# Performance work log

Hardware: AMD Instinct MI355X
Metric: run time of the kernel (lower is better)

The kernel has to match this reference:

```python
import jax, jax.numpy as jnp
import numpy as np
from jax import lax

B, L, H, E, V = 16, 128, 1024, 512, 32000
MAX_LENGTH = 128
SOS_INDEX = 1
NUM_LAYERS = 2


def setup_inputs() -> dict:
    key = jax.random.key(0)
    ks = jax.random.split(key, 16)
    inp = {}
    inp['input_tensor'] = jax.random.randint(ks[0], (B, L), 0, V)
    inp['target_tensor'] = jax.random.randint(ks[1], (B, L), 0, V)
    inp['true_sample'] = 1
    s = lambda k, shape, fan: jax.random.normal(k, shape, jnp.float32) / np.float32(np.sqrt(fan))
    inp['embedding'] = jax.random.normal(ks[2], (V, E), jnp.float32) * 0.02
    inp['enc_W'] = s(ks[3], (E, H), E)
    inp['enc_b'] = jnp.zeros((H,), jnp.float32)
    inp['Wih0'] = s(ks[4], (E, 3 * H), E)
    inp['Whh0'] = s(ks[5], (H, 3 * H), H)
    inp['bih0'] = jnp.zeros((3 * H,), jnp.float32)
    inp['bhh0'] = jnp.zeros((3 * H,), jnp.float32)
    inp['Wih1'] = s(ks[6], (H, 3 * H), H)
    inp['Whh1'] = s(ks[7], (H, 3 * H), H)
    inp['bih1'] = jnp.zeros((3 * H,), jnp.float32)
    inp['bhh1'] = jnp.zeros((3 * H,), jnp.float32)
    inp['W_out'] = s(ks[8], (2 * H, V), 2 * H)
    inp['b_out'] = jnp.zeros((V,), jnp.float32)
    return inp


def _gru_cell(x, h, Wih, Whh, bih, bhh):
    gx = x @ Wih + bih
    gh = h @ Whh + bhh
    xr, xz, xn = jnp.split(gx, 3, axis=-1)
    hr, hz, hn = jnp.split(gh, 3, axis=-1)
    r = jax.nn.sigmoid(xr + hr)
    z = jax.nn.sigmoid(xz + hz)
    n = jnp.tanh(xn + r * hn)
    return (1.0 - z) * n + z * h


def _forward(input_tensor, true_sample, embedding, enc_W, enc_b,
             Wih0, Whh0, bih0, bhh0, Wih1, Whh1, bih1, bhh1, W_out, b_out):
    batch_size, input_length = input_tensor.shape
    target_length = input_length
    # Encoder: embed + per-timestep projection -> [B, L, H]
    enc_emb = embedding[input_tensor]
    enc_hidden = jnp.tanh(enc_emb @ enc_W + enc_b)
    enc_hidden_t = jnp.transpose(enc_hidden, (1, 0, 2))  # [L, B, H]
    # Pad at the front to max_length (mirrors the copy loop)
    encoder_outputs = jnp.zeros((MAX_LENGTH, batch_size, H), enc_hidden.dtype)
    encoder_outputs = encoder_outputs.at[MAX_LENGTH - input_length:].set(enc_hidden_t)
    # Decoder initial hidden: last encoder state stacked over layers
    h_init = enc_hidden_t[-1]  # [B, H]
    # NOTE: original never updates decoder_input inside the loop -> constant SOS
    x0 = jnp.broadcast_to(embedding[SOS_INDEX], (batch_size, E))
    inv_sqrt_h = np.float32(1.0 / np.sqrt(H))

    def step(carry, _):
        h0, h1 = carry
        h0 = _gru_cell(x0, h0, Wih0, Whh0, bih0, bhh0)
        h1 = _gru_cell(h0, h1, Wih1, Whh1, bih1, bhh1)
        scores = jnp.einsum('bh,lbh->bl', h1, encoder_outputs) * inv_sqrt_h
        attn = jax.nn.softmax(scores, axis=-1)
        ctx = jnp.einsum('bl,lbh->bh', attn, encoder_outputs)
        logits = jnp.concatenate([h1, ctx], axis=-1) @ W_out + b_out
        return (h0, h1), jax.nn.sigmoid(logits)

    _, probs = lax.scan(step, (h_init, h_init), None, length=target_length)
    decoder_outputs = jnp.transpose(probs, (1, 0, 2))  # [B, T, V]
    # Scalar gather: p[b,w] = decoder_outputs[b, w, input_tensor[b, w]]
    out_probabilities = jnp.take_along_axis(decoder_outputs, input_tensor[..., None], axis=2)[..., 0]
    target = jnp.full(input_tensor.shape, np.float32(int(true_sample)), jnp.float32)
    p = jnp.clip(out_probabilities, 1e-12, 1.0 - 1e-7)
    bce = -(target * jnp.log(p) + (1.0 - target) * jnp.log1p(-p))
    loss = jnp.mean(bce) / np.float32(batch_size)
    return loss, out_probabilities


def reference(input_tensor, target_tensor, true_sample, embedding, enc_W, enc_b,
              Wih0, Whh0, bih0, bhh0, Wih1, Whh1, bih1, bhh1, W_out, b_out):
    return _forward(input_tensor, true_sample, embedding, enc_W, enc_b,
                    Wih0, Whh0, bih0, bhh0, Wih1, Whh1, bih1, bhh1, W_out, b_out)
```

## Files before the change

### kernel.cpp

```cpp
#include <hip/hip_runtime.h>
#include <math.h>

#define BB 16
#define LL 128
#define HH 1024
#define EE 512
#define VV 32000
#define G3 3072
#define NBLK 256

__device__ __forceinline__ float sigmoidf_(float x){ return 1.0f/(1.0f+expf(-x)); }

__device__ __forceinline__ float red64(float v){
  v += __shfl_xor(v, 1, 64); v += __shfl_xor(v, 2, 64);
  v += __shfl_xor(v, 4, 64); v += __shfl_xor(v, 8, 64);
  v += __shfl_xor(v, 16, 64); v += __shfl_xor(v, 32, 64);
  return v;
}
__device__ __forceinline__ float red32(float v){
  v += __shfl_xor(v, 1, 64); v += __shfl_xor(v, 2, 64);
  v += __shfl_xor(v, 4, 64); v += __shfl_xor(v, 8, 64);
  v += __shfl_xor(v, 16, 64);
  return v;
}

__global__ void k_rowidx(const int* __restrict__ inp, int* __restrict__ idx){
  int r = blockIdx.x*256 + threadIdx.x;
  if (r < 2048){ int l = r >> 4, b = r & 15; idx[r] = inp[b*LL + l]; }
}

template<int ACT, int KK>
__global__ __launch_bounds__(256) void k_gemm(const float* __restrict__ A, const int* __restrict__ rowidx,
                       const float* __restrict__ Bm, const float* __restrict__ bias,
                       float* __restrict__ C, int N){
  constexpr int KS = (KK==512)?9:10;
  __shared__ float As[32*KK];
  const int tid = threadIdx.x;
  const int r0 = blockIdx.x*32;
  const int c  = blockIdx.y*512 + (tid<<1);
  for (int i = tid; i < 32*KK; i += 256){
    int rr = i >> KS;
    int row = r0 + rr;
    int arow = rowidx ? rowidx[row] : row;
    int kk = i - (rr<<KS);
    As[i] = A[(size_t)arow*KK + kk];
  }
  __syncthreads();
  float2 acc[32];
  #pragma unroll
  for (int r=0;r<32;r++){ acc[r].x=0.f; acc[r].y=0.f; }
  for (int k=0;k<KK;k++){
    const float2 w = *(const float2*)(Bm + (size_t)k*N + c);
    #pragma unroll
    for (int r=0;r<32;r++){
      float a = As[(r<<KS)+k];
      acc[r].x = fmaf(a,w.x,acc[r].x);
      acc[r].y = fmaf(a,w.y,acc[r].y);
    }
  }
  const float2 bv = *(const float2*)(bias + c);
  #pragma unroll
  for (int r=0;r<32;r++){
    float x = acc[r].x + bv.x, y = acc[r].y + bv.y;
    if (ACT==1){ x = tanhf(x); y = tanhf(y); }
    *(float2*)(C + (size_t)(r0+r)*N + c) = make_float2(x,y);
  }
}

__global__ __launch_bounds__(512,1) void k_chains(
    const float* enclast, float* H0all, float* H1all,
    const float* __restrict__ Whh0, const float* __restrict__ Whh1,
    const float* __restrict__ Wih0, const float* __restrict__ Wih1,
    const float* __restrict__ emb,
    const float* __restrict__ bih0, const float* __restrict__ bhh0,
    const float* __restrict__ bhh1, const float* __restrict__ bih1,
    int* flags, int* go)
{
  __shared__ float w0l[12][1024];
  __shared__ float w1l[12][1024];
  __shared__ float wil[12][1024];
  __shared__ float gxbuf[16*12];
  const int tid  = threadIdx.x;
  const int jb   = blockIdx.x << 2;
  const int waveid = tid >> 6;
  const int cgA = waveid >> 2;
  const int bgA = waveid & 3;
  const int kgA = tid & 63;
  const int koffA = kgA << 2;
  const int b0A = bgA << 2;
  const int cgB = waveid >> 1;
  const int bgB = ((waveid & 1) << 1) | ((tid >> 5) & 1);
  const int kgB = tid & 31;
  const int koffB = kgB << 2;
  const int b0B = bgB << 2;
  const int mB  = cgB >> 1;

  const bool pwA = (kgA < 8);
  const int  jlA = (cgA << 1) + (kgA & 1);
  const int  jpA = jb + jlA;
  const int  biA = (kgA >> 1) & 3;
  const int  bA  = b0A + biA;
  const bool pwB = (cgB >= 2) && (kgB < 8);
  const int  jlB = ((cgB & 1) << 1) + (kgB & 1);
  const int  jpB = jb + jlB;
  const int  biB = (kgB >> 1) & 3;
  const int  bB  = b0B + biB;

  float g0r=0.f, g0z=0.f, g0n=0.f;
  {
    for (int idx = tid; idx < 1536; idx += 512){
      int g = idx >> 9, k = idx & 511;
      float4 a = *(const float4*)(Wih0 + (size_t)k*G3 + g*1024 + jb);
      w0l[g*4+0][k]=a.x; w0l[g*4+1][k]=a.y; w0l[g*4+2][k]=a.z; w0l[g*4+3][k]=a.w;
    }
    __syncthreads();
    const float* e1 = emb + EE;
    float ag[6];
    #pragma unroll
    for (int cl=0;cl<6;cl++) ag[cl]=0.f;
    #pragma unroll
    for (int u=0;u<2;u++){
      float4 e = *(const float4*)(e1 + u*256 + koffA);
      #pragma unroll
      for (int cl=0;cl<6;cl++){
        const int gc = ((cl>>1)<<2) + (cgA<<1) + (cl&1);
        const float4 w = *(const float4*)(&w0l[gc][u*256 + koffA]);
        float v = ag[cl];
        v=fmaf(w.x,e.x,v); v=fmaf(w.y,e.y,v); v=fmaf(w.z,e.z,v); v=fmaf(w.w,e.w,v);
        ag[cl]=v;
      }
    }
    #pragma unroll
    for (int cl=0;cl<6;cl++) ag[cl] = red64(ag[cl]);
    if (pwA){
      const int jj = kgA & 1;
      g0r = (jj ? ag[1] : ag[0]) + bih0[jpA];
      g0z = (jj ? ag[3] : ag[2]) + bih0[1024+jpA];
      g0n = (jj ? ag[5] : ag[4]) + bih0[2048+jpA];
    }
    __syncthreads();
  }

  for (int idx = tid; idx < 3072; idx += 512){
    int g = idx >> 10, k = idx & 1023;
    float4 a = *(const float4*)(Whh0 + (size_t)k*G3 + g*1024 + jb);
    w0l[g*4+0][k]=a.x; w0l[g*4+1][k]=a.y; w0l[g*4+2][k]=a.z; w0l[g*4+3][k]=a.w;
    float4 d = *(const float4*)(Whh1 + (size_t)k*G3 + g*1024 + jb);
    w1l[g*4+0][k]=d.x; w1l[g*4+1][k]=d.y; w1l[g*4+2][k]=d.z; w1l[g*4+3][k]=d.w;
    float4 e = *(const float4*)(Wih1 + (size_t)k*G3 + g*1024 + jb);
    wil[g*4+0][k]=e.x; wil[g*4+1][k]=e.y; wil[g*4+2][k]=e.z; wil[g*4+3][k]=e.w;
  }
  float b0rA=0.f,b0zA=0.f,b0nA=0.f;
  if (pwA){ b0rA = bhh0[jpA]; b0zA = bhh0[1024+jpA]; b0nA = bhh0[2048+jpA]; }
  float birB=0.f,bizB=0.f,binB=0.f,b1rB=0.f,b1zB=0.f,b1nB=0.f;
  if (pwB){
    birB = bih1[jpB]; bizB = bih1[1024+jpB]; binB = bih1[2048+jpB];
    b1rB = bhh1[jpB]; b1zB = bhh1[1024+jpB]; b1nB = bhh1[2048+jpB];
  }
  __syncthreads();

  const int myflag = (int)blockIdx.x * 32;

  for (int t = 0; t <= LL; ++t){
    if (t >= 1){
      if (blockIdx.x == 0){
        if (tid < 256){
          while (__hip_atomic_load(&flags[tid*32], __ATOMIC_RELAXED,
                                   __HIP_MEMORY_SCOPE_AGENT) < t)
            __builtin_amdgcn_s_sleep(1);
        }
        __syncthreads();
        if (tid == 0)
          __hip_atomic_store(go, t, __ATOMIC_RELAXED, __HIP_MEMORY_SCOPE_AGENT);
      } else {
        if (tid == 0){
          while (__hip_atomic_load(go, __ATOMIC_RELAXED,
                                   __HIP_MEMORY_SCOPE_AGENT) < t)
            __builtin_amdgcn_s_sleep(1);
        }
        __syncthreads();
      }
    }

    if (t >= 1){
      const float* hp0 = H0all + (size_t)(t-1)*(BB*HH);
      const float* hp1 = (t==1) ? enclast : (H1all + (size_t)(t-2)*(BB*HH));
      const float* hr  = mB ? hp1 : hp0;
      float hprev1 = 0.f;
      if (pwB) hprev1 = hp1[(size_t)bB*HH + jpB];

      float accB[6][4];
      #pragma unroll
      for (int cl=0;cl<6;cl++)
        #pragma unroll
        for (int bi=0;bi<4;bi++) accB[cl][bi]=0.f;

      #pragma unroll
      for (int u=0;u<8;u++){
        float4 h4[4];
        #pragma unroll
        for (int bi=0;bi<4;bi++)
          h4[bi] = *(const float4*)(hr + (size_t)(b0B+bi)*HH + u*128 + koffB);
        #pragma unroll
        for (int cl=0;cl<6;cl++){
          const int gc = ((cl>>1)<<2) + ((cgB&1)<<1) + (cl&1);
          const float4 w = mB ? *(const float4*)(&w1l[gc][u*128 + koffB])
                              : *(const float4*)(&wil[gc][u*128 + koffB]);
          #pragma unroll
          for (int bi=0;bi<4;bi++){
            float v = accB[cl][bi];
            v=fmaf(w.x,h4[bi].x,v); v=fmaf(w.y,h4[bi].y,v);
            v=fmaf(w.z,h4[bi].z,v); v=fmaf(w.w,h4[bi].w,v);
            accB[cl][bi]=v;
          }
        }
      }
      #pragma unroll
      for (int cl=0;cl<6;cl++)
        #pragma unroll
        for (int bi=0;bi<4;bi++) accB[cl][bi] = red32(accB[cl][bi]);

      if (mB == 0){
        #pragma unroll
        for (int cl=0;cl<6;cl++){
          if (kgB == cl){
            const int g = cl >> 1;
            const int jl = ((cgB&1)<<1) + (cl&1);
            #pragma unroll
            for (int bi=0;bi<4;bi++)
              gxbuf[(b0B+bi)*12 + g*4 + jl] = accB[cl][bi];
          }
        }
      }
      __syncthreads();
      if (pwB){
        float ghr=0.f, ghz=0.f, ghn=0.f;
        #pragma unroll
        for (int jj=0;jj<2;jj++)
          #pragma unroll
          for (int ii=0;ii<4;ii++){
            bool sel = ((kgB&1)==jj) & (biB==ii);
            ghr = sel ? accB[jj][ii]   : ghr;
            ghz = sel ? accB[2+jj][ii] : ghz;
            ghn = sel ? accB[4+jj][ii] : ghn;
          }
        float gxr = gxbuf[bB*12 + 0*4 + jlB];
        float gxz = gxbuf[bB*12 + 1*4 + jlB];
        float gxn = gxbuf[bB*12 + 2*4 + jlB];
        float r = sigmoidf_(gxr + birB + ghr + b1rB);
        float z = sigmoidf_(gxz + bizB + ghz + b1zB);
        float n = tanhf    (gxn + binB + r*(ghn + b1nB));
        float hnew = (1.f-z)*n + z*hprev1;
        __hip_atomic_store((int*)&H1all[(size_t)(t-1)*(BB*HH) + (size_t)bB*HH + jpB],
                           __float_as_int(hnew),
                           __ATOMIC_RELAXED, __HIP_MEMORY_SCOPE_AGENT);
      }
    }

    if (t < LL){
      const float* hp0 = (t==0) ? enclast : (H0all + (size_t)(t-1)*(BB*HH));
      float hprev0 = 0.f;
      if (pwA) hprev0 = hp0[(size_t)bA*HH + jpA];

      float acc0[6][4];
      #pragma unroll
      for (int cl=0;cl<6;cl++)
        #pragma unroll
        for (int bi=0;bi<4;bi++) acc0[cl][bi]=0.f;

      #pragma unroll
      for (int u=0;u<4;u++){
        float4 h4[4];
        #pragma unroll
        for (int bi=0;bi<4;bi++)
          h4[bi] = *(const float4*)(hp0 + (size_t)(b0A+bi)*HH + u*256 + koffA);
        #pragma unroll
        for (int cl=0;cl<6;cl++){
          const int gc = ((cl>>1)<<2) + (cgA<<1) + (cl&1);
          const float4 w = *(const float4*)(&w0l[gc][u*256 + koffA]);
          #pragma unroll
          for (int bi=0;bi<4;bi++){
            float v = acc0[cl][bi];
            v=fmaf(w.x,h4[bi].x,v); v=fmaf(w.y,h4[bi].y,v);
            v=fmaf(w.z,h4[bi].z,v); v=fmaf(w.w,h4[bi].w,v);
            acc0[cl][bi]=v;
          }
        }
      }
      #pragma unroll
      for (int cl=0;cl<6;cl++)
        #pragma unroll
        for (int bi=0;bi<4;bi++) acc0[cl][bi] = red64(acc0[cl][bi]);

      if (pwA){
        float ghr=0.f, ghz=0.f, ghn=0.f;
        #pragma unroll
        for (int jj=0;jj<2;jj++)
          #pragma unroll
          for (int ii=0;ii<4;ii++){
            bool sel = ((kgA&1)==jj) & (biA==ii);
            ghr = sel ? acc0[jj][ii]   : ghr;
            ghz = sel ? acc0[2+jj][ii] : ghz;
            ghn = sel ? acc0[4+jj][ii] : ghn;
          }
        float r = sigmoidf_(g0r + ghr + b0rA);
        float z = sigmoidf_(g0z + ghz + b0zA);
        float n = tanhf    (g0n + r*(ghn + b0nA));
        float hnew = (1.f-z)*n + z*hprev0;
        __hip_atomic_store((int*)&H0all[(size_t)t*(BB*HH) + (size_t)bA*HH + jpA],
                           __float_as_int(hnew),
                           __ATOMIC_RELAXED, __HIP_MEMORY_SCOPE_AGENT);
      }
    }

    if (t < LL){
      asm volatile("s_waitcnt vmcnt(0)" ::: "memory");
      __syncthreads();
      if (tid == 0)
        __hip_atomic_store(&flags[myflag], t+1,
                           __ATOMIC_RELAXED, __HIP_MEMORY_SCOPE_AGENT);
    }
  }
}

__global__ __launch_bounds__(256) void k_attn(const float* __restrict__ enc, const float* __restrict__ H1,
                       float* __restrict__ ctx){
  __shared__ float h1s[8][HH];
  __shared__ float sc[8][LL];
  __shared__ float part[2][8][LL];
  const int tid = threadIdx.x;
  const int s0 = blockIdx.x*8, b = blockIdx.y;
  for (int i = tid; i < 8*HH; i += 256){
    int si = i >> 10, k = i & 1023;
    h1s[si][k] = H1[(size_t)(s0+si)*BB*HH + (size_t)b*HH + k];
  }
  __syncthreads();
  {
    const int l = tid & 127, half = tid >> 7;
    const float4* er = (const float4*)(enc + ((size_t)l*BB + b)*HH + half*512);
    float a[8];
    #pragma unroll
    for (int s=0;s<8;s++) a[s]=0.f;
    for (int q=0;q<128;q++){
      float4 e = er[q];
      #pragma unroll
      for (int s=0;s<8;s++){
        const float4 h = *(const float4*)(&h1s[s][half*512 + q*4]);
        a[s] += h.x*e.x + h.y*e.y + h.z*e.z + h.w*e.w;
      }
    }
    #pragma unroll
    for (int s=0;s<8;s++) part[half][s][l] = a[s];
  }
  __syncthreads();
  for (int p = tid; p < 1024; p += 256){
    int s = p >> 7, l = p & 127;
    sc[s][l] = (part[0][s][l] + part[1][s][l]) * 0.03125f;
  }
  __syncthreads();
  {
    int s = tid >> 5, lid = tid & 31;
    float v0 = sc[s][lid], v1 = sc[s][lid+32], v2 = sc[s][lid+64], v3 = sc[s][lid+96];
    float m = fmaxf(fmaxf(v0,v1),fmaxf(v2,v3));
    for (int off=16; off>=1; off>>=1) m = fmaxf(m, __shfl_xor(m, off, 32));
    float e0=__expf(v0-m), e1=__expf(v1-m), e2=__expf(v2-m), e3=__expf(v3-m);
    float ssum = e0+e1+e2+e3;
    for (int off=16; off>=1; off>>=1) ssum += __shfl_xor(ssum, off, 32);
    float inv = 1.0f/ssum;
    sc[s][lid]=e0*inv; sc[s][lid+32]=e1*inv; sc[s][lid+64]=e2*inv; sc[s][lid+96]=e3*inv;
  }
  __syncthreads();
  {
    float acc[4][8];
    #pragma unroll
    for (int q=0;q<4;q++)
      #pragma unroll
      for (int s=0;s<8;s++) acc[q][s]=0.f;
    for (int l=0;l<128;l++){
      const float* er = enc + ((size_t)l*BB + b)*HH + tid;
      float a[8];
      #pragma unroll
      for (int s=0;s<8;s++) a[s] = sc[s][l];
      #pragma unroll
      for (int q=0;q<4;q++){
        float e = er[q*256];
        #pragma unroll
        for (int s=0;s<8;s++) acc[q][s] = fmaf(a[s], e, acc[q][s]);
      }
    }
    #pragma unroll
    for (int s=0;s<8;s++)
      #pragma unroll
      for (int q=0;q<4;q++)
        ctx[(size_t)(s0+s)*BB*HH + (size_t)b*HH + tid + q*256] = acc[q][s];
  }
}

__global__ __launch_bounds__(256) void k_logit(const float* __restrict__ H1, const float* __restrict__ ctx,
                        const float* __restrict__ Wout, const float* __restrict__ bout,
                        const int* __restrict__ inp, const int* __restrict__ ts,
                        float* __restrict__ outp, float* __restrict__ bce){
  __shared__ float rbuf[256];
  const int i = blockIdx.x;
  const int b = i >> 7, t = i & 127;
  const int v = inp[b*LL + t];
  const int tid = threadIdx.x;
  const float* h1r = H1 + ((size_t)t*BB + b)*HH;
  const float* cxr = ctx + ((size_t)t*BB + b)*HH;
  float acc = 0.f;
  #pragma unroll
  for (int q=0;q<4;q++){
    int k = tid + q*256;
    acc = fmaf(h1r[k], Wout[(size_t)k*VV + v], acc);
  }
  #pragma unroll
  for (int q=0;q<4;q++){
    int k = tid + q*256;
    acc = fmaf(cxr[k], Wout[(size_t)(k+1024)*VV + v], acc);
  }
  rbuf[tid] = acc;
  __syncthreads();
  for (int s=128; s>0; s>>=1){
    if (tid < s) rbuf[tid] += rbuf[tid+s];
    __syncthreads();
  }
  if (tid==0){
    float logit = rbuf[0] + bout[v];
    float p = 1.0f/(1.0f + expf(-logit));
    outp[b*LL + t] = p;
    float pc = fminf(fmaxf(p, 1e-12f), 1.0f - 1e-7f);
    float tg = (float)ts[0];
    bce[i] = -(tg*logf(pc) + (1.0f-tg)*log1pf(-pc));
  }
}

__global__ void k_loss(const float* __restrict__ bce, float* __restrict__ out0){
  __shared__ float rbuf[256];
  int tid = threadIdx.x;
  float s = 0.f;
  for (int i = tid; i < 2048; i += 256) s += bce[i];
  rbuf[tid] = s; __syncthreads();
  for (int st=128; st>0; st>>=1){
    if (tid<st) rbuf[tid]+=rbuf[tid+st];
    __syncthreads();
  }
  if (tid==0) out0[0] = rbuf[0] * (1.0f/(2048.0f*16.0f));
}

extern "C" void kernel_launch(void* const* d_in, const int* in_sizes, int n_in,
                              void* d_out, int out_size, void* d_ws, size_t ws_size,
                              hipStream_t stream){
  (void)in_sizes; (void)n_in; (void)out_size; (void)ws_size;
  const int*   inp   = (const int*)d_in[0];
  const int*   ts    = (const int*)d_in[2];
  const float* emb   = (const float*)d_in[3];
  const float* encW  = (const float*)d_in[4];
  const float* encb  = (const float*)d_in[5];
  const float* Wih0  = (const float*)d_in[6];
  const float* Whh0  = (const float*)d_in[7];
  const float* bih0  = (const float*)d_in[8];
  const float* bhh0  = (const float*)d_in[9];
  const float* Wih1  = (const float*)d_in[10];
  const float* Whh1  = (const float*)d_in[11];
  const float* bih1  = (const float*)d_in[12];
  const float* bhh1  = (const float*)d_in[13];
  const float* Wout  = (const float*)d_in[14];
  const float* bout  = (const float*)d_in[15];
  float* out = (float*)d_out;

  float* ws      = (float*)d_ws;
  float* enc_out = ws;
  float* H0      = enc_out + 2097152;
  float* H1      = H0 + 2097152;
  float* GX1     = H1 + 2097152;
  float* CTX     = GX1 + 6291456;
  float* gx0     = CTX + 2097152;
  float* bceb    = gx0 + 3072;
  int*   rowidx  = (int*)(bceb + 2048);
  int*   flags   = rowidx + 2048;
  int*   go      = flags + 256*32;

  hipMemsetAsync(flags, 0, (256*32 + 32)*sizeof(int), stream);
  k_rowidx<<<8,256,0,stream>>>(inp, rowidx);
  k_gemm<1,512><<<dim3(64,2),256,0,stream>>>(emb, rowidx, encW, encb, enc_out, HH);

  const float* enclast = enc_out + (size_t)127*BB*HH;

  k_chains<<<NBLK,512,0,stream>>>(enclast, H0, H1, Whh0, Whh1, Wih0, Wih1, emb,
                                  bih0, bhh0, bhh1, bih1, flags, go);
  k_attn<<<dim3(16,16),256,0,stream>>>(enc_out, H1, CTX);
  k_logit<<<2048,256,0,stream>>>(H1, CTX, Wout, bout, inp, ts, out+1, bceb);
  k_loss<<<1,256,0,stream>>>(bceb, out);
}
```

Before: 2.070 ms.

## Store recurrent GRU weights as packed fp16 in LDS and use dot2 with 1024 threads

The persistent recurrent kernel now converts Whh0, Whh1, Wih1 and Wih0 slices to packed half pairs in shared memory. It computes the gate dot products with v_dot2_f32_f16, with hidden states also packed to fp16 on the fly. The block size doubles to 1024 threads and the work is remapped so each wave covers fewer batch rows per layer-0 group, halving LDS footprint and per-thread register accumulators. This targets the per-step latency of the serial 128-step chain, but it reduces precision of the recurrent matmuls to fp16 inputs, which may drift over many steps.

```diff
diff --git a/kernel.cpp b/kernel.cpp
--- a/kernel.cpp
+++ b/kernel.cpp
@@ -8,19 +8,24 @@
 #define VV 32000
 #define G3 3072
 #define NBLK 256
+#define KP 576
+
+typedef __fp16 h2t __attribute__((ext_vector_type(2)));
+typedef unsigned int uint_;
 
 __device__ __forceinline__ float sigmoidf_(float x){ return 1.0f/(1.0f+expf(-x)); }
 
+__device__ __forceinline__ uint_ pk16(float a, float b){
+  h2t h = __builtin_amdgcn_cvt_pkrtz(a, b);
+  return __builtin_bit_cast(uint_, h);
+}
+__device__ __forceinline__ void dot2(float& acc, uint_ w, uint_ h){
+  asm("v_dot2_f32_f16 %0, %1, %2, %0" : "+v"(acc) : "v"(w), "v"(h));
+}
 __device__ __forceinline__ float red64(float v){
   v += __shfl_xor(v, 1, 64); v += __shfl_xor(v, 2, 64);
   v += __shfl_xor(v, 4, 64); v += __shfl_xor(v, 8, 64);
   v += __shfl_xor(v, 16, 64); v += __shfl_xor(v, 32, 64);
-  return v;
-}
-__device__ __forceinline__ float red32(float v){
-  v += __shfl_xor(v, 1, 64); v += __shfl_xor(v, 2, 64);
-  v += __shfl_xor(v, 4, 64); v += __shfl_xor(v, 8, 64);
-  v += __shfl_xor(v, 16, 64);
   return v;
 }
 
@@ -67,7 +72,7 @@
   }
 }
 
-__global__ __launch_bounds__(512,1) void k_chains(
+__global__ __launch_bounds__(1024,1) void k_chains(
     const float* enclast, float* H0all, float* H1all,
     const float* __restrict__ Whh0, const float* __restrict__ Whh1,
     const float* __restrict__ Wih0, const float* __restrict__ Wih1,
@@ -76,42 +81,44 @@
     const float* __restrict__ bhh1, const float* __restrict__ bih1,
     int* flags, int* go)
 {
-  __shared__ float w0l[12][1024];
-  __shared__ float w1l[12][1024];
-  __shared__ float wil[12][1024];
+  __shared__ uint_ w0l[12][KP];
+  __shared__ uint_ w1l[12][KP];
+  __shared__ uint_ wil[12][KP];
   __shared__ float gxbuf[16*12];
   const int tid  = threadIdx.x;
   const int jb   = blockIdx.x << 2;
   const int waveid = tid >> 6;
-  const int cgA = waveid >> 2;
-  const int bgA = waveid & 3;
-  const int kgA = tid & 63;
-  const int koffA = kgA << 2;
-  const int b0A = bgA << 2;
-  const int cgB = waveid >> 1;
-  const int bgB = ((waveid & 1) << 1) | ((tid >> 5) & 1);
-  const int kgB = tid & 31;
-  const int koffB = kgB << 2;
+  const int lane = tid & 63;
+  const int cgA = waveid >> 3;
+  const int bgA = waveid & 7;
+  const int b0A = bgA << 1;
+  const int cgB = waveid >> 2;
+  const int mB  = cgB >> 1;
+  const int bgB = waveid & 3;
   const int b0B = bgB << 2;
-  const int mB  = cgB >> 1;
-
-  const bool pwA = (kgA < 8);
-  const int  jlA = (cgA << 1) + (kgA & 1);
+  const int koff = lane << 2;
+
+  const bool pwA = (lane < 4);
+  const int  jlA = (cgA << 1) + (lane & 1);
   const int  jpA = jb + jlA;
-  const int  biA = (kgA >> 1) & 3;
+  const int  biA = (lane >> 1) & 1;
   const int  bA  = b0A + biA;
-  const bool pwB = (cgB >= 2) && (kgB < 8);
-  const int  jlB = ((cgB & 1) << 1) + (kgB & 1);
+  const bool pwB = (mB == 1) && (lane < 8);
+  const int  jlB = ((cgB & 1) << 1) + (lane & 1);
   const int  jpB = jb + jlB;
-  const int  biB = (kgB >> 1) & 3;
+  const int  biB = (lane >> 1) & 3;
   const int  bB  = b0B + biB;
 
   float g0r=0.f, g0z=0.f, g0n=0.f;
   {
-    for (int idx = tid; idx < 1536; idx += 512){
-      int g = idx >> 9, k = idx & 511;
-      float4 a = *(const float4*)(Wih0 + (size_t)k*G3 + g*1024 + jb);
-      w0l[g*4+0][k]=a.x; w0l[g*4+1][k]=a.y; w0l[g*4+2][k]=a.z; w0l[g*4+3][k]=a.w;
+    for (int idx = tid; idx < 768; idx += 1024){
+      int g = idx >> 8, kp = idx & 255, k = kp << 1;
+      float4 a0 = *(const float4*)(Wih0 + (size_t)k*G3 + g*1024 + jb);
+      float4 a1 = *(const float4*)(Wih0 + (size_t)(k+1)*G3 + g*1024 + jb);
+      w0l[g*4+0][kp] = pk16(a0.x, a1.x);
+      w0l[g*4+1][kp] = pk16(a0.y, a1.y);
+      w0l[g*4+2][kp] = pk16(a0.z, a1.z);
+      w0l[g*4+3][kp] = pk16(a0.w, a1.w);
     }
     __syncthreads();
     const float* e1 = emb + EE;
@@ -120,20 +127,20 @@
     for (int cl=0;cl<6;cl++) ag[cl]=0.f;
     #pragma unroll
     for (int u=0;u<2;u++){
-      float4 e = *(const float4*)(e1 + u*256 + koffA);
+      const int k0 = u*256 + koff, kp0 = (k0 >> 1);
+      float4 e = *(const float4*)(e1 + k0);
+      uint_ e01 = pk16(e.x, e.y), e23 = pk16(e.z, e.w);
       #pragma unroll
       for (int cl=0;cl<6;cl++){
         const int gc = ((cl>>1)<<2) + (cgA<<1) + (cl&1);
-        const float4 w = *(const float4*)(&w0l[gc][u*256 + koffA]);
-        float v = ag[cl];
-        v=fmaf(w.x,e.x,v); v=fmaf(w.y,e.y,v); v=fmaf(w.z,e.z,v); v=fmaf(w.w,e.w,v);
-        ag[cl]=v;
+        dot2(ag[cl], w0l[gc][kp0],   e01);
+        dot2(ag[cl], w0l[gc][kp0+1], e23);
       }
     }
     #pragma unroll
     for (int cl=0;cl<6;cl++) ag[cl] = red64(ag[cl]);
     if (pwA){
-      const int jj = kgA & 1;
+      const int jj = lane & 1;
       g0r = (jj ? ag[1] : ag[0]) + bih0[jpA];
       g0z = (jj ? ag[3] : ag[2]) + bih0[1024+jpA];
       g0n = (jj ? ag[5] : ag[4]) + bih0[2048+jpA];
@@ -141,14 +148,32 @@
     __syncthreads();
   }
 
-  for (int idx = tid; idx < 3072; idx += 512){
-    int g = idx >> 10, k = idx & 1023;
-    float4 a = *(const float4*)(Whh0 + (size_t)k*G3 + g*1024 + jb);
-    w0l[g*4+0][k]=a.x; w0l[g*4+1][k]=a.y; w0l[g*4+2][k]=a.z; w0l[g*4+3][k]=a.w;
-    float4 d = *(const float4*)(Whh1 + (size_t)k*G3 + g*1024 + jb);
-    w1l[g*4+0][k]=d.x; w1l[g*4+1][k]=d.y; w1l[g*4+2][k]=d.z; w1l[g*4+3][k]=d.w;
-    float4 e = *(const float4*)(Wih1 + (size_t)k*G3 + g*1024 + jb);
-    wil[g*4+0][k]=e.x; wil[g*4+1][k]=e.y; wil[g*4+2][k]=e.z; wil[g*4+3][k]=e.w;
+  for (int idx = tid; idx < 1536; idx += 1024){
+    int g = idx >> 9, kp = idx & 511, k = kp << 1;
+    {
+      float4 a0 = *(const float4*)(Whh0 + (size_t)k*G3 + g*1024 + jb);
+      float4 a1 = *(const float4*)(Whh0 + (size_t)(k+1)*G3 + g*1024 + jb);
+      w0l[g*4+0][kp] = pk16(a0.x, a1.x);
+      w0l[g*4+1][kp] = pk16(a0.y, a1.y);
+      w0l[g*4+2][kp] = pk16(a0.z, a1.z);
+      w0l[g*4+3][kp] = pk16(a0.w, a1.w);
+    }
+    {
+      float4 a0 = *(const float4*)(Whh1 + (size_t)k*G3 + g*1024 + jb);
+      float4 a1 = *(const float4*)(Whh1 + (size_t)(k+1)*G3 + g*1024 + jb);
+      w1l[g*4+0][kp] = pk16(a0.x, a1.x);
+      w1l[g*4+1][kp] = pk16(a0.y, a1.y);
+      w1l[g*4+2][kp] = pk16(a0.z, a1.z);
+      w1l[g*4+3][kp] = pk16(a0.w, a1.w);
+    }
+    {
+      float4 a0 = *(const float4*)(Wih1 + (size_t)k*G3 + g*1024 + jb);
+      float4 a1 = *(const float4*)(Wih1 + (size_t)(k+1)*G3 + g*1024 + jb);
+      wil[g*4+0][kp] = pk16(a0.x, a1.x);
+      wil[g*4+1][kp] = pk16(a0.y, a1.y);
+      wil[g*4+2][kp] = pk16(a0.z, a1.z);
+      wil[g*4+3][kp] = pk16(a0.w, a1.w);
+    }
   }
   float b0rA=0.f,b0zA=0.f,b0nA=0.f;
   if (pwA){ b0rA = bhh0[jpA]; b0zA = bhh0[1024+jpA]; b0nA = bhh0[2048+jpA]; }
@@ -196,34 +221,36 @@
         for (int bi=0;bi<4;bi++) accB[cl][bi]=0.f;
 
       #pragma unroll
-      for (int u=0;u<8;u++){
-        float4 h4[4];
-        #pragma unroll
-        for (int bi=0;bi<4;bi++)
-          h4[bi] = *(const float4*)(hr + (size_t)(b0B+bi)*HH + u*128 + koffB);
+      for (int u=0;u<4;u++){
+        const int k0 = u*256 + koff, kp0 = (k0 >> 1);
+        uint_ hh[4][2];
+        #pragma unroll
+        for (int bi=0;bi<4;bi++){
+          float4 hv = *(const float4*)(hr + (size_t)(b0B+bi)*HH + k0);
+          hh[bi][0] = pk16(hv.x, hv.y);
+          hh[bi][1] = pk16(hv.z, hv.w);
+        }
         #pragma unroll
         for (int cl=0;cl<6;cl++){
           const int gc = ((cl>>1)<<2) + ((cgB&1)<<1) + (cl&1);
-          const float4 w = mB ? *(const float4*)(&w1l[gc][u*128 + koffB])
-                              : *(const float4*)(&wil[gc][u*128 + koffB]);
+          const uint_ w01 = mB ? w1l[gc][kp0]   : wil[gc][kp0];
+          const uint_ w23 = mB ? w1l[gc][kp0+1] : wil[gc][kp0+1];
           #pragma unroll
           for (int bi=0;bi<4;bi++){
-            float v = accB[cl][bi];
-            v=fmaf(w.x,h4[bi].x,v); v=fmaf(w.y,h4[bi].y,v);
-            v=fmaf(w.z,h4[bi].z,v); v=fmaf(w.w,h4[bi].w,v);
-            accB[cl][bi]=v;
+            dot2(accB[cl][bi], w01, hh[bi][0]);
+            dot2(accB[cl][bi], w23, hh[bi][1]);
           }
         }
       }
       #pragma unroll
       for (int cl=0;cl<6;cl++)
         #pragma unroll
-        for (int bi=0;bi<4;bi++) accB[cl][bi] = red32(accB[cl][bi]);
+        for (int bi=0;bi<4;bi++) accB[cl][bi] = red64(accB[cl][bi]);
 
       if (mB == 0){
         #pragma unroll
         for (int cl=0;cl<6;cl++){
-          if (kgB == cl){
+          if (lane == cl){
             const int g = cl >> 1;
             const int jl = ((cgB&1)<<1) + (cl&1);
             #pragma unroll
@@ -239,14 +266,14 @@
         for (int jj=0;jj<2;jj++)
           #pragma unroll
           for (int ii=0;ii<4;ii++){
-            bool sel = ((kgB&1)==jj) & (biB==ii);
+            bool sel = ((lane&1)==jj) & (biB==ii);
             ghr = sel ? accB[jj][ii]   : ghr;
             ghz = sel ? accB[2+jj][ii] : ghz;
             ghn = sel ? accB[4+jj][ii] : ghn;
           }
-        float gxr = gxbuf[bB*12 + 0*4 + jlB];
-        float gxz = gxbuf[bB*12 + 1*4 + jlB];
-        float gxn = gxbuf[bB*12 + 2*4 + jlB];
+        float gxr = gxbuf[bB*12 + 0 + jlB];
+        float gxz = gxbuf[bB*12 + 4 + jlB];
+        float gxn = gxbuf[bB*12 + 8 + jlB];
         float r = sigmoidf_(gxr + birB + ghr + b1rB);
         float z = sigmoidf_(gxz + bizB + ghz + b1zB);
         float n = tanhf    (gxn + binB + r*(ghn + b1nB));
@@ -262,43 +289,45 @@
       float hprev0 = 0.f;
       if (pwA) hprev0 = hp0[(size_t)bA*HH + jpA];
 
-      float acc0[6][4];
-      #pragma unroll
-      for (int cl=0;cl<6;cl++)
-        #pragma unroll
-        for (int bi=0;bi<4;bi++) acc0[cl][bi]=0.f;
+      float acc0[6][2];
+      #pragma unroll
+      for (int cl=0;cl<6;cl++){ acc0[cl][0]=0.f; acc0[cl][1]=0.f; }
 
       #pragma unroll
       for (int u=0;u<4;u++){
-        float4 h4[4];
-        #pragma unroll
-        for (int bi=0;bi<4;bi++)
-          h4[bi] = *(const float4*)(hp0 + (size_t)(b0A+bi)*HH + u*256 + koffA);
+        const int k0 = u*256 + koff, kp0 = (k0 >> 1);
+        uint_ hh[2][2];
+        #pragma unroll
+        for (int bi=0;bi<2;bi++){
+          float4 hv = *(const float4*)(hp0 + (size_t)(b0A+bi)*HH + k0);
+          hh[bi][0] = pk16(hv.x, hv.y);
+          hh[bi][1] = pk16(hv.z, hv.w);
+        }
         #pragma unroll
         for (int cl=0;cl<6;cl++){
           const int gc = ((cl>>1)<<2) + (cgA<<1) + (cl&1);
-          const float4 w = *(const float4*)(&w0l[gc][u*256 + koffA]);
+          const uint_ w01 = w0l[gc][kp0];
+          const uint_ w23 = w0l[gc][kp0+1];
           #pragma unroll
-          for (int bi=0;bi<4;bi++){
-            float v = acc0[cl][bi];
-            v=fmaf(w.x,h4[bi].x,v); v=fmaf(w.y,h4[bi].y,v);
-            v=fmaf(w.z,h4[bi].z,v); v=fmaf(w.w,h4[bi].w,v);
-            acc0[cl][bi]=v;
+          for (int bi=0;bi<2;bi++){
+            dot2(acc0[cl][bi], w01, hh[bi][0]);
+            dot2(acc0[cl][bi], w23, hh[bi][1]);
           }
         }
       }
       #pragma unroll
-      for (int cl=0;cl<6;cl++)
-        #pragma unroll
-        for (int bi=0;bi<4;bi++) acc0[cl][bi] = red64(acc0[cl][bi]);
+      for (int cl=0;cl<6;cl++){
+        acc0[cl][0] = red64(acc0[cl][0]);
+        acc0[cl][1] = red64(acc0[cl][1]);
+      }
 
       if (pwA){
         float ghr=0.f, ghz=0.f, ghn=0.f;
         #pragma unroll
         for (int jj=0;jj<2;jj++)
           #pragma unroll
-          for (int ii=0;ii<4;ii++){
-            bool sel = ((kgA&1)==jj) & (biA==ii);
+          for (int ii=0;ii<2;ii++){
+            bool sel = ((lane&1)==jj) & (biA==ii);
             ghr = sel ? acc0[jj][ii]   : ghr;
             ghz = sel ? acc0[2+jj][ii] : ghz;
             ghn = sel ? acc0[4+jj][ii] : ghn;
@@ -480,14 +509,14 @@
   int*   flags   = rowidx + 2048;
   int*   go      = flags + 256*32;
 
-  hipMemsetAsync(flags, 0, (256*32 + 32)*sizeof(int), stream);
+  (void)hipMemsetAsync(flags, 0, (256*32 + 32)*sizeof(int), stream);
   k_rowidx<<<8,256,0,stream>>>(inp, rowidx);
   k_gemm<1,512><<<dim3(64,2),256,0,stream>>>(emb, rowidx, encW, encb, enc_out, HH);
 
   const float* enclast = enc_out + (size_t)127*BB*HH;
 
-  k_chains<<<NBLK,512,0,stream>>>(enclast, H0, H1, Whh0, Whh1, Wih0, Wih1, emb,
-                                  bih0, bhh0, bhh1, bih1, flags, go);
+  k_chains<<<NBLK,1024,0,stream>>>(enclast, H0, H1, Whh0, Whh1, Wih0, Wih1, emb,
+                                   bih0, bhh0, bhh1, bih1, flags, go);
   k_attn<<<dim3(16,16),256,0,stream>>>(enc_out, H1, CTX);
   k_logit<<<2048,256,0,stream>>>(H1, CTX, Wout, bout, inp, ts, out+1, bceb);
   k_loss<<<1,256,0,stream>>>(bceb, out);
```

Result: slower. 2.812 ms (+35.9%).

## Split GRU layers into separate persistent block groups with fp16 dot2 for layer 1

Applied to the files above, without the earlier changes.

The persistent recurrence kernel is split into two groups of 256 blocks. One group runs layer 0 and the other runs layer 1, each with its own flag/go barrier, and layer 1 trails layer 0 by one step via the layer-0 go counter. Layer-1 weights are packed to fp16 pairs in shared memory and multiplied with v_dot2_f32_f16, so Wih1 and Whh1 fit in one 48 KB buffer alongside the layer split. The aim is to shorten the per-step critical path and shrink LDS per block so more blocks fit. The cost is lower precision in layer 1 and a dependence on all 512 blocks being co-resident, which risks deadlock.

```diff
diff --git a/kernel.cpp b/kernel.cpp
--- a/kernel.cpp
+++ b/kernel.cpp
@@ -9,8 +9,18 @@
 #define G3 3072
 #define NBLK 256
 
+typedef __fp16 h2t __attribute__((ext_vector_type(2)));
+typedef unsigned int uint_;
+
 __device__ __forceinline__ float sigmoidf_(float x){ return 1.0f/(1.0f+expf(-x)); }
 
+__device__ __forceinline__ uint_ pk16(float a, float b){
+  h2t h = __builtin_amdgcn_cvt_pkrtz(a, b);
+  return __builtin_bit_cast(uint_, h);
+}
+__device__ __forceinline__ void dot2(float& acc, uint_ w, uint_ h){
+  asm("v_dot2_f32_f16 %0, %1, %2, %0" : "+v"(acc) : "v"(w), "v"(h));
+}
 __device__ __forceinline__ float red64(float v){
   v += __shfl_xor(v, 1, 64); v += __shfl_xor(v, 2, 64);
   v += __shfl_xor(v, 4, 64); v += __shfl_xor(v, 8, 64);
@@ -74,117 +84,236 @@
     const float* __restrict__ emb,
     const float* __restrict__ bih0, const float* __restrict__ bhh0,
     const float* __restrict__ bhh1, const float* __restrict__ bih1,
-    int* flags, int* go)
+    int* flagsA, int* flagsB, int* goA, int* goB)
 {
-  __shared__ float w0l[12][1024];
-  __shared__ float w1l[12][1024];
-  __shared__ float wil[12][1024];
+  __shared__ uint_ wbuf[12][1024];
   __shared__ float gxbuf[16*12];
-  const int tid  = threadIdx.x;
-  const int jb   = blockIdx.x << 2;
+  float (*wf)[1024] = (float(*)[1024])wbuf;
+  const int tid = threadIdx.x;
   const int waveid = tid >> 6;
-  const int cgA = waveid >> 2;
-  const int bgA = waveid & 3;
-  const int kgA = tid & 63;
-  const int koffA = kgA << 2;
-  const int b0A = bgA << 2;
-  const int cgB = waveid >> 1;
-  const int bgB = ((waveid & 1) << 1) | ((tid >> 5) & 1);
-  const int kgB = tid & 31;
-  const int koffB = kgB << 2;
-  const int b0B = bgB << 2;
-  const int mB  = cgB >> 1;
-
-  const bool pwA = (kgA < 8);
-  const int  jlA = (cgA << 1) + (kgA & 1);
-  const int  jpA = jb + jlA;
-  const int  biA = (kgA >> 1) & 3;
-  const int  bA  = b0A + biA;
-  const bool pwB = (cgB >= 2) && (kgB < 8);
-  const int  jlB = ((cgB & 1) << 1) + (kgB & 1);
-  const int  jpB = jb + jlB;
-  const int  biB = (kgB >> 1) & 3;
-  const int  bB  = b0B + biB;
-
-  float g0r=0.f, g0z=0.f, g0n=0.f;
-  {
+  const bool isA = (blockIdx.x < NBLK);
+  const int bx = isA ? (int)blockIdx.x : ((int)blockIdx.x - NBLK);
+  const int jb = bx << 2;
+
+  if (isA){
+    const int cgA = waveid >> 2;
+    const int bgA = waveid & 3;
+    const int kgA = tid & 63;
+    const int koffA = kgA << 2;
+    const int b0A = bgA << 2;
+    const bool pwA = (kgA < 8);
+    const int jlA = (cgA << 1) + (kgA & 1);
+    const int jpA = jb + jlA;
+    const int biA = (kgA >> 1) & 3;
+    const int bA  = b0A + biA;
+
+    float g0r=0.f, g0z=0.f, g0n=0.f;
+    {
+      for (int idx = tid; idx < 1536; idx += 512){
+        int g = idx >> 9, k = idx & 511;
+        float4 a = *(const float4*)(Wih0 + (size_t)k*G3 + g*1024 + jb);
+        wf[g*4+0][k]=a.x; wf[g*4+1][k]=a.y; wf[g*4+2][k]=a.z; wf[g*4+3][k]=a.w;
+      }
+      __syncthreads();
+      const float* e1 = emb + EE;
+      float ag[6];
+      #pragma unroll
+      for (int cl=0;cl<6;cl++) ag[cl]=0.f;
+      #pragma unroll
+      for (int u=0;u<2;u++){
+        float4 e = *(const float4*)(e1 + u*256 + koffA);
+        #pragma unroll
+        for (int cl=0;cl<6;cl++){
+          const int gc = ((cl>>1)<<2) + (cgA<<1) + (cl&1);
+          const float4 w = *(const float4*)(&wf[gc][u*256 + koffA]);
+          float v = ag[cl];
+          v=fmaf(w.x,e.x,v); v=fmaf(w.y,e.y,v); v=fmaf(w.z,e.z,v); v=fmaf(w.w,e.w,v);
+          ag[cl]=v;
+        }
+      }
+      #pragma unroll
+      for (int cl=0;cl<6;cl++) ag[cl] = red64(ag[cl]);
+      if (pwA){
+        const int jj = kgA & 1;
+        g0r = (jj ? ag[1] : ag[0]) + bih0[jpA];
+        g0z = (jj ? ag[3] : ag[2]) + bih0[1024+jpA];
+        g0n = (jj ? ag[5] : ag[4]) + bih0[2048+jpA];
+      }
+      __syncthreads();
+    }
+    for (int idx = tid; idx < 3072; idx += 512){
+      int g = idx >> 10, k = idx & 1023;
+      float4 a = *(const float4*)(Whh0 + (size_t)k*G3 + g*1024 + jb);
+      wf[g*4+0][k]=a.x; wf[g*4+1][k]=a.y; wf[g*4+2][k]=a.z; wf[g*4+3][k]=a.w;
+    }
+    float b0rA=0.f,b0zA=0.f,b0nA=0.f;
+    if (pwA){ b0rA = bhh0[jpA]; b0zA = bhh0[1024+jpA]; b0nA = bhh0[2048+jpA]; }
+    __syncthreads();
+
+    const int myflag = bx * 32;
+    for (int t = 0; t < LL; ++t){
+      if (t >= 1){
+        if (blockIdx.x == 0){
+          if (tid < 256){
+            while (__hip_atomic_load(&flagsA[tid*32], __ATOMIC_RELAXED,
+                                     __HIP_MEMORY_SCOPE_AGENT) < t)
+              __builtin_amdgcn_s_sleep(1);
+          }
+          __syncthreads();
+          if (tid == 0)
+            __hip_atomic_store(goA, t, __ATOMIC_RELAXED, __HIP_MEMORY_SCOPE_AGENT);
+        } else {
+          if (tid == 0){
+            while (__hip_atomic_load(goA, __ATOMIC_RELAXED,
+                                     __HIP_MEMORY_SCOPE_AGENT) < t)
+              __builtin_amdgcn_s_sleep(1);
+          }
+          __syncthreads();
+        }
+      }
+      const float* hp0 = (t==0) ? enclast : (H0all + (size_t)(t-1)*(BB*HH));
+      float hprev0 = 0.f;
+      if (pwA) hprev0 = hp0[(size_t)bA*HH + jpA];
+
+      float acc0[6][4];
+      #pragma unroll
+      for (int cl=0;cl<6;cl++)
+        #pragma unroll
+        for (int bi=0;bi<4;bi++) acc0[cl][bi]=0.f;
+      #pragma unroll
+      for (int u=0;u<4;u++){
+        float4 h4[4];
+        #pragma unroll
+        for (int bi=0;bi<4;bi++)
+          h4[bi] = *(const float4*)(hp0 + (size_t)(b0A+bi)*HH + u*256 + koffA);
+        #pragma unroll
+        for (int cl=0;cl<6;cl++){
+          const int gc = ((cl>>1)<<2) + (cgA<<1) + (cl&1);
+          const float4 w = *(const float4*)(&wf[gc][u*256 + koffA]);
+          #pragma unroll
+          for (int bi=0;bi<4;bi++){
+            float v = acc0[cl][bi];
+            v=fmaf(w.x,h4[bi].x,v); v=fmaf(w.y,h4[bi].y,v);
+            v=fmaf(w.z,h4[bi].z,v); v=fmaf(w.w,h4[bi].w,v);
+            acc0[cl][bi]=v;
+          }
+        }
+      }
+      #pragma unroll
+      for (int cl=0;cl<6;cl++)
+        #pragma unroll
+        for (int bi=0;bi<4;bi++) acc0[cl][bi] = red64(acc0[cl][bi]);
+
+      if (pwA){
+        float ghr=0.f, ghz=0.f, ghn=0.f;
+        #pragma unroll
+        for (int jj=0;jj<2;jj++)
+          #pragma unroll
+          for (int ii=0;ii<4;ii++){
+            bool sel = ((kgA&1)==jj) & (biA==ii);
+            ghr = sel ? acc0[jj][ii]   : ghr;
+            ghz = sel ? acc0[2+jj][ii] : ghz;
+            ghn = sel ? acc0[4+jj][ii] : ghn;
+          }
+        float r = sigmoidf_(g0r + ghr + b0rA);
+        float z = sigmoidf_(g0z + ghz + b0zA);
+        float n = tanhf    (g0n + r*(ghn + b0nA));
+        float hnew = (1.f-z)*n + z*hprev0;
+        __hip_atomic_store((int*)&H0all[(size_t)t*(BB*HH) + (size_t)bA*HH + jpA],
+                           __float_as_int(hnew),
+                           __ATOMIC_RELAXED, __HIP_MEMORY_SCOPE_AGENT);
+      }
+      asm volatile("s_waitcnt vmcnt(0)" ::: "memory");
+      __syncthreads();
+      if (tid == 0)
+        __hip_atomic_store(&flagsA[myflag], t+1,
+                           __ATOMIC_RELAXED, __HIP_MEMORY_SCOPE_AGENT);
+    }
+    if (blockIdx.x == 0){
+      if (tid < 256){
+        while (__hip_atomic_load(&flagsA[tid*32], __ATOMIC_RELAXED,
+                                 __HIP_MEMORY_SCOPE_AGENT) < LL)
+          __builtin_amdgcn_s_sleep(1);
+      }
+      __syncthreads();
+      if (tid == 0)
+        __hip_atomic_store(goA, LL, __ATOMIC_RELAXED, __HIP_MEMORY_SCOPE_AGENT);
+    }
+  } else {
+    const int cgB = waveid >> 1;
+    const int bgB = ((waveid & 1) << 1) | ((tid >> 5) & 1);
+    const int kgB = tid & 31;
+    const int koffB = kgB << 2;
+    const int b0B = bgB << 2;
+    const int mB  = cgB >> 1;
+    const bool pwB = (mB == 1) && (kgB < 8);
+    const int  jlB = ((cgB & 1) << 1) + (kgB & 1);
+    const int  jpB = jb + jlB;
+    const int  biB = (kgB >> 1) & 3;
+    const int  bB  = b0B + biB;
+    const int  wbase = mB ? 512 : 0;
+
     for (int idx = tid; idx < 1536; idx += 512){
-      int g = idx >> 9, k = idx & 511;
-      float4 a = *(const float4*)(Wih0 + (size_t)k*G3 + g*1024 + jb);
-      w0l[g*4+0][k]=a.x; w0l[g*4+1][k]=a.y; w0l[g*4+2][k]=a.z; w0l[g*4+3][k]=a.w;
+      int g = idx >> 9, kp = idx & 511, k = kp << 1;
+      {
+        float4 a0 = *(const float4*)(Wih1 + (size_t)k*G3 + g*1024 + jb);
+        float4 a1 = *(const float4*)(Wih1 + (size_t)(k+1)*G3 + g*1024 + jb);
+        wbuf[g*4+0][kp] = pk16(a0.x, a1.x);
+        wbuf[g*4+1][kp] = pk16(a0.y, a1.y);
+        wbuf[g*4+2][kp] = pk16(a0.z, a1.z);
+        wbuf[g*4+3][kp] = pk16(a0.w, a1.w);
+      }
+      {
+        float4 a0 = *(const float4*)(Whh1 + (size_t)k*G3 + g*1024 + jb);
+        float4 a1 = *(const float4*)(Whh1 + (size_t)(k+1)*G3 + g*1024 + jb);
+        wbuf[g*4+0][512+kp] = pk16(a0.x, a1.x);
+        wbuf[g*4+1][512+kp] = pk16(a0.y, a1.y);
+        wbuf[g*4+2][512+kp] = pk16(a0.z, a1.z);
+        wbuf[g*4+3][512+kp] = pk16(a0.w, a1.w);
+      }
+    }
+    float birB=0.f,bizB=0.f,binB=0.f,b1rB=0.f,b1zB=0.f,b1nB=0.f;
+    if (pwB){
+      birB = bih1[jpB]; bizB = bih1[1024+jpB]; binB = bih1[2048+jpB];
+      b1rB = bhh1[jpB]; b1zB = bhh1[1024+jpB]; b1nB = bhh1[2048+jpB];
     }
     __syncthreads();
-    const float* e1 = emb + EE;
-    float ag[6];
-    #pragma unroll
-    for (int cl=0;cl<6;cl++) ag[cl]=0.f;
-    #pragma unroll
-    for (int u=0;u<2;u++){
-      float4 e = *(const float4*)(e1 + u*256 + koffA);
-      #pragma unroll
-      for (int cl=0;cl<6;cl++){
-        const int gc = ((cl>>1)<<2) + (cgA<<1) + (cl&1);
-        const float4 w = *(const float4*)(&w0l[gc][u*256 + koffA]);
-        float v = ag[cl];
-        v=fmaf(w.x,e.x,v); v=fmaf(w.y,e.y,v); v=fmaf(w.z,e.z,v); v=fmaf(w.w,e.w,v);
-        ag[cl]=v;
-      }
-    }
-    #pragma unroll
-    for (int cl=0;cl<6;cl++) ag[cl] = red64(ag[cl]);
-    if (pwA){
-      const int jj = kgA & 1;
-      g0r = (jj ? ag[1] : ag[0]) + bih0[jpA];
-      g0z = (jj ? ag[3] : ag[2]) + bih0[1024+jpA];
-      g0n = (jj ? ag[5] : ag[4]) + bih0[2048+jpA];
-    }
-    __syncthreads();
-  }
-
-  for (int idx = tid; idx < 3072; idx += 512){
-    int g = idx >> 10, k = idx & 1023;
-    float4 a = *(const float4*)(Whh0 + (size_t)k*G3 + g*1024 + jb);
-    w0l[g*4+0][k]=a.x; w0l[g*4+1][k]=a.y; w0l[g*4+2][k]=a.z; w0l[g*4+3][k]=a.w;
-    float4 d = *(const float4*)(Whh1 + (size_t)k*G3 + g*1024 + jb);
-    w1l[g*4+0][k]=d.x; w1l[g*4+1][k]=d.y; w1l[g*4+2][k]=d.z; w1l[g*4+3][k]=d.w;
-    float4 e = *(const float4*)(Wih1 + (size_t)k*G3 + g*1024 + jb);
-    wil[g*4+0][k]=e.x; wil[g*4+1][k]=e.y; wil[g*4+2][k]=e.z; wil[g*4+3][k]=e.w;
-  }
-  float b0rA=0.f,b0zA=0.f,b0nA=0.f;
-  if (pwA){ b0rA = bhh0[jpA]; b0zA = bhh0[1024+jpA]; b0nA = bhh0[2048+jpA]; }
-  float birB=0.f,bizB=0.f,binB=0.f,b1rB=0.f,b1zB=0.f,b1nB=0.f;
-  if (pwB){
-    birB = bih1[jpB]; bizB = bih1[1024+jpB]; binB = bih1[2048+jpB];
-    b1rB = bhh1[jpB]; b1zB = bhh1[1024+jpB]; b1nB = bhh1[2048+jpB];
-  }
-  __syncthreads();
-
-  const int myflag = (int)blockIdx.x * 32;
-
-  for (int t = 0; t <= LL; ++t){
-    if (t >= 1){
-      if (blockIdx.x == 0){
-        if (tid < 256){
-          while (__hip_atomic_load(&flags[tid*32], __ATOMIC_RELAXED,
-                                   __HIP_MEMORY_SCOPE_AGENT) < t)
+
+    const int myflag = bx * 32;
+    for (int t = 0; t < LL; ++t){
+      if (blockIdx.x == NBLK){
+        if (t >= 1){
+          if (tid < 256){
+            while (__hip_atomic_load(&flagsB[tid*32], __ATOMIC_RELAXED,
+                                     __HIP_MEMORY_SCOPE_AGENT) < t)
+              __builtin_amdgcn_s_sleep(1);
+          }
+          __syncthreads();
+          if (tid == 0)
+            __hip_atomic_store(goB, t, __ATOMIC_RELAXED, __HIP_MEMORY_SCOPE_AGENT);
+        }
+        if (tid == 0){
+          while (__hip_atomic_load(goA, __ATOMIC_RELAXED,
+                                   __HIP_MEMORY_SCOPE_AGENT) < t+1)
             __builtin_amdgcn_s_sleep(1);
         }
         __syncthreads();
-        if (tid == 0)
-          __hip_atomic_store(go, t, __ATOMIC_RELAXED, __HIP_MEMORY_SCOPE_AGENT);
       } else {
         if (tid == 0){
-          while (__hip_atomic_load(go, __ATOMIC_RELAXED,
-                                   __HIP_MEMORY_SCOPE_AGENT) < t)
+          if (t >= 1){
+            while (__hip_atomic_load(goB, __ATOMIC_RELAXED,
+                                     __HIP_MEMORY_SCOPE_AGENT) < t)
+              __builtin_amdgcn_s_sleep(1);
+          }
+          while (__hip_atomic_load(goA, __ATOMIC_RELAXED,
+                                   __HIP_MEMORY_SCOPE_AGENT) < t+1)
             __builtin_amdgcn_s_sleep(1);
         }
         __syncthreads();
       }
-    }
-
-    if (t >= 1){
-      const float* hp0 = H0all + (size_t)(t-1)*(BB*HH);
-      const float* hp1 = (t==1) ? enclast : (H1all + (size_t)(t-2)*(BB*HH));
+
+      const float* hp0 = H0all + (size_t)t*(BB*HH);
+      const float* hp1 = (t==0) ? enclast : (H1all + (size_t)(t-1)*(BB*HH));
       const float* hr  = mB ? hp1 : hp0;
       float hprev1 = 0.f;
       if (pwB) hprev1 = hp1[(size_t)bB*HH + jpB];
@@ -197,21 +326,24 @@
 
       #pragma unroll
       for (int u=0;u<8;u++){
-        float4 h4[4];
-        #pragma unroll
-        for (int bi=0;bi<4;bi++)
-          h4[bi] = *(const float4*)(hr + (size_t)(b0B+bi)*HH + u*128 + koffB);
+        const int k0 = u*128 + koffB;
+        const int kp0 = wbase + (k0 >> 1);
+        uint_ hh[4][2];
+        #pragma unroll
+        for (int bi=0;bi<4;bi++){
+          float4 hv = *(const float4*)(hr + (size_t)(b0B+bi)*HH + k0);
+          hh[bi][0] = pk16(hv.x, hv.y);
+          hh[bi][1] = pk16(hv.z, hv.w);
+        }
         #pragma unroll
         for (int cl=0;cl<6;cl++){
           const int gc = ((cl>>1)<<2) + ((cgB&1)<<1) + (cl&1);
-          const float4 w = mB ? *(const float4*)(&w1l[gc][u*128 + koffB])
-                              : *(const float4*)(&wil[gc][u*128 + koffB]);
+          const uint_ w01 = wbuf[gc][kp0];
+          const uint_ w23 = wbuf[gc][kp0+1];
           #pragma unroll
           for (int bi=0;bi<4;bi++){
-            float v = accB[cl][bi];
-            v=fmaf(w.x,h4[bi].x,v); v=fmaf(w.y,h4[bi].y,v);
-            v=fmaf(w.z,h4[bi].z,v); v=fmaf(w.w,h4[bi].w,v);
-            accB[cl][bi]=v;
+            dot2(accB[cl][bi], w01, hh[bi][0]);
+            dot2(accB[cl][bi], w23, hh[bi][1]);
           }
         }
       }
@@ -244,80 +376,21 @@
             ghz = sel ? accB[2+jj][ii] : ghz;
             ghn = sel ? accB[4+jj][ii] : ghn;
           }
-        float gxr = gxbuf[bB*12 + 0*4 + jlB];
-        float gxz = gxbuf[bB*12 + 1*4 + jlB];
-        float gxn = gxbuf[bB*12 + 2*4 + jlB];
+        float gxr = gxbuf[bB*12 + 0 + jlB];
+        float gxz = gxbuf[bB*12 + 4 + jlB];
+        float gxn = gxbuf[bB*12 + 8 + jlB];
         float r = sigmoidf_(gxr + birB + ghr + b1rB);
         float z = sigmoidf_(gxz + bizB + ghz + b1zB);
         float n = tanhf    (gxn + binB + r*(ghn + b1nB));
         float hnew = (1.f-z)*n + z*hprev1;
-        __hip_atomic_store((int*)&H1all[(size_t)(t-1)*(BB*HH) + (size_t)bB*HH + jpB],
+        __hip_atomic_store((int*)&H1all[(size_t)t*(BB*HH) + (size_t)bB*HH + jpB],
                            __float_as_int(hnew),
                            __ATOMIC_RELAXED, __HIP_MEMORY_SCOPE_AGENT);
       }
-    }
-
-    if (t < LL){
-      const float* hp0 = (t==0) ? enclast : (H0all + (size_t)(t-1)*(BB*HH));
-      float hprev0 = 0.f;
-      if (pwA) hprev0 = hp0[(size_t)bA*HH + jpA];
-
-      float acc0[6][4];
-      #pragma unroll
-      for (int cl=0;cl<6;cl++)
-        #pragma unroll
-        for (int bi=0;bi<4;bi++) acc0[cl][bi]=0.f;
-
-      #pragma unroll
-      for (int u=0;u<4;u++){
-        float4 h4[4];
-        #pragma unroll
-        for (int bi=0;bi<4;bi++)
-          h4[bi] = *(const float4*)(hp0 + (size_t)(b0A+bi)*HH + u*256 + koffA);
-        #pragma unroll
-        for (int cl=0;cl<6;cl++){
-          const int gc = ((cl>>1)<<2) + (cgA<<1) + (cl&1);
-          const float4 w = *(const float4*)(&w0l[gc][u*256 + koffA]);
-          #pragma unroll
-          for (int bi=0;bi<4;bi++){
-            float v = acc0[cl][bi];
-            v=fmaf(w.x,h4[bi].x,v); v=fmaf(w.y,h4[bi].y,v);
-            v=fmaf(w.z,h4[bi].z,v); v=fmaf(w.w,h4[bi].w,v);
-            acc0[cl][bi]=v;
-          }
-        }
-      }
-      #pragma unroll
-      for (int cl=0;cl<6;cl++)
-        #pragma unroll
-        for (int bi=0;bi<4;bi++) acc0[cl][bi] = red64(acc0[cl][bi]);
-
-      if (pwA){
-        float ghr=0.f, ghz=0.f, ghn=0.f;
-        #pragma unroll
-        for (int jj=0;jj<2;jj++)
-          #pragma unroll
-          for (int ii=0;ii<4;ii++){
-            bool sel = ((kgA&1)==jj) & (biA==ii);
-            ghr = sel ? acc0[jj][ii]   : ghr;
-            ghz = sel ? acc0[2+jj][ii] : ghz;
-            ghn = sel ? acc0[4+jj][ii] : ghn;
-          }
-        float r = sigmoidf_(g0r + ghr + b0rA);
-        float z = sigmoidf_(g0z + ghz + b0zA);
-        float n = tanhf    (g0n + r*(ghn + b0nA));
-        float hnew = (1.f-z)*n + z*hprev0;
-        __hip_atomic_store((int*)&H0all[(size_t)t*(BB*HH) + (size_t)bA*HH + jpA],
-                           __float_as_int(hnew),
-                           __ATOMIC_RELAXED, __HIP_MEMORY_SCOPE_AGENT);
-      }
-    }
-
-    if (t < LL){
       asm volatile("s_waitcnt vmcnt(0)" ::: "memory");
       __syncthreads();
       if (tid == 0)
-        __hip_atomic_store(&flags[myflag], t+1,
+        __hip_atomic_store(&flagsB[myflag], t+1,
                            __ATOMIC_RELAXED, __HIP_MEMORY_SCOPE_AGENT);
     }
   }
@@ -477,17 +550,19 @@
   float* gx0     = CTX + 2097152;
   float* bceb    = gx0 + 3072;
   int*   rowidx  = (int*)(bceb + 2048);
-  int*   flags   = rowidx + 2048;
-  int*   go      = flags + 256*32;
-
-  hipMemsetAsync(flags, 0, (256*32 + 32)*sizeof(int), stream);
+  int*   flagsA  = rowidx + 2048;
+  int*   flagsB  = flagsA + 256*32;
+  int*   goA     = flagsB + 256*32;
+  int*   goB     = goA + 32;
+
+  (void)hipMemsetAsync(flagsA, 0, (512*32 + 64)*sizeof(int), stream);
   k_rowidx<<<8,256,0,stream>>>(inp, rowidx);
   k_gemm<1,512><<<dim3(64,2),256,0,stream>>>(emb, rowidx, encW, encb, enc_out, HH);
 
   const float* enclast = enc_out + (size_t)127*BB*HH;
 
-  k_chains<<<NBLK,512,0,stream>>>(enclast, H0, H1, Whh0, Whh1, Wih0, Wih1, emb,
-                                  bih0, bhh0, bhh1, bih1, flags, go);
+  k_chains<<<2*NBLK,512,0,stream>>>(enclast, H0, H1, Whh0, Whh1, Wih0, Wih1, emb,
+                                    bih0, bhh0, bhh1, bih1, flagsA, flagsB, goA, goB);
   k_attn<<<dim3(16,16),256,0,stream>>>(enc_out, H1, CTX);
   k_logit<<<2048,256,0,stream>>>(H1, CTX, Wout, bout, inp, ts, out+1, bceb);
   k_loss<<<1,256,0,stream>>>(bceb, out);
```

Result: slower. 2.669 ms (+29.0%).
